# Kernel optimization log

Hardware: AMD Instinct MI355X
Metric: run time of the kernel (lower is better)

## Reference

```python
import jax, jax.numpy as jnp
from jax import lax
import numpy as np

C, CK, CV, K = 256, 32, 32, 3  # channels, key_channels, value_channels, kernel_size
B, H, W = 8, 128, 128


def setup_inputs() -> dict:
    key = jax.random.key(0)
    ks = jax.random.split(key, 12)
    s = 0.05
    return {
        "x": jax.random.normal(ks[0], (B, C, H, W), jnp.float32),
        # key branch: 1x1 conv C->CK (+ReLU), depthwise 3x3 CK->CK, 1x1 conv CK->K*K
        "k1_w": jax.random.normal(ks[1], (CK, C), jnp.float32) * s,
        "k1_b": jax.random.normal(ks[2], (CK,), jnp.float32) * s,
        "dw_w": jax.random.normal(ks[3], (CK, 1, K, K), jnp.float32) * s,
        "dw_b": jax.random.normal(ks[4], (CK,), jnp.float32) * s,
        "k3_w": jax.random.normal(ks[5], (K * K, CK), jnp.float32) * s,
        "k3_b": jax.random.normal(ks[6], (K * K,), jnp.float32) * s,
        # value branch: 1x1 conv C->CV (no act)
        "v_w": jax.random.normal(ks[7], (CV, C), jnp.float32) * s,
        "v_b": jax.random.normal(ks[8], (CV,), jnp.float32) * s,
        # out conv: 1x1 CV->C (no act)
        "o_w": jax.random.normal(ks[9], (C, CV), jnp.float32) * s,
        "o_b": jax.random.normal(ks[10], (C,), jnp.float32) * s,
    }


def _conv1x1(t, w, b):
    # t: [B,Cin,H,W], w: [Cout,Cin] -> [B,Cout,H,W]
    return jnp.einsum("bchw,oc->bohw", t, w) + b[None, :, None, None]


def reference(x, k1_w, k1_b, dw_w, dw_b, k3_w, k3_b, v_w, v_b, o_w, o_b):
    b, _, h, w = x.shape
    pad = (K - 1) // 2
    # ---- key branch ----
    k = jax.nn.relu(_conv1x1(x, k1_w, k1_b))
    k = lax.conv_general_dilated(
        k, dw_w, window_strides=(1, 1), padding=[(pad, pad), (pad, pad)],
        dimension_numbers=("NCHW", "OIHW", "NCHW"), feature_group_count=CK,
    ) + dw_b[None, :, None, None]
    k = _conv1x1(k, k3_w, k3_b)                      # [B, K*K, H, W]
    weights = jax.nn.softmax(k, axis=1)[:, None]     # [B, 1, K*K, H, W]
    # ---- value branch: 1x1 conv then unfold (3x3 neighborhoods, pad 1) ----
    v = _conv1x1(x, v_w, v_b)                        # [B, CV, H, W]
    vp = jnp.pad(v, ((0, 0), (0, 0), (pad, pad), (pad, pad)))
    # torch Unfold ordering: per-channel, kernel offsets row-major
    patches = jnp.stack(
        [vp[:, :, i : i + h, j : j + w] for i in range(K) for j in range(K)],
        axis=2,
    )                                                # [B, CV, K*K, H, W]
    y = jnp.sum(weights * patches, axis=2)           # [B, CV, H, W]
    y = _conv1x1(y, o_w, o_b)                        # [B, C, H, W]
    return x + y
```

## Files before the change

kernel.cpp:

```cpp
#include <hip/hip_runtime.h>
#include <cmath>

namespace {
constexpr int Cc = 256, CKc = 32, CVc = 32, KKc = 9;
constexpr int Bc = 8, Hc = 128, Wc = 128, HWc = Hc * Wc;

typedef __attribute__((ext_vector_type(8))) short   s16x8;
typedef __attribute__((ext_vector_type(8))) __bf16  bf16x8;
typedef __attribute__((ext_vector_type(4))) float   f32x4;

__device__ inline unsigned short f2bf(float f) {
    union { float f; unsigned u; } v; v.f = f;
    unsigned u = v.u + 0x7fffu + ((v.u >> 16) & 1u);
    return (unsigned short)(u >> 16);
}
}

__global__ __launch_bounds__(256) void ns_k1v(
    const float* __restrict__ x,
    const float* __restrict__ k1_w, const float* __restrict__ k1_b,
    const float* __restrict__ v_w,  const float* __restrict__ v_b,
    const float* __restrict__ o_w,
    unsigned short* __restrict__ k1pm, unsigned short* __restrict__ vpm,
    unsigned short* __restrict__ owbf)
{
    constexpr int LP = 72;
    __shared__ short w_bf[64][LP];
    __shared__ short x_bf[128][LP];

    const int tid = threadIdx.x;
    const int l   = tid & 63;
    const int li  = l & 15;
    const int lk  = l >> 4;
    const int wv  = __builtin_amdgcn_readfirstlane(tid >> 6);

    if (blockIdx.x == 0) {
        for (int i = tid * 4; i < Cc * CVc; i += 256 * 4) {
            const float4 f = *(const float4*)(o_w + i);
            const unsigned a = (unsigned)f2bf(f.x) | ((unsigned)f2bf(f.y) << 16);
            const unsigned c = (unsigned)f2bf(f.z) | ((unsigned)f2bf(f.w) << 16);
            *(uint2*)(owbf + i) = make_uint2(a, c);
        }
    }

    const int flat0 = blockIdx.x * 128;
    const int b  = flat0 / HWc;
    const int pp = flat0 - b * HWc;
    const float* xb = x + (size_t)b * Cc * HWc + pp;

    const int sp2 = (tid & 63) * 2;
    const int scg = tid >> 6;
    const int so   = tid & 63;
    const int swc0 = (tid >> 6) * 16;
    const float* wsrc = (so < 32) ? (k1_w + (size_t)so * Cc)
                                  : (v_w + (size_t)(so - 32) * Cc);

    f32x4 acc[8];
    const f32x4 zero = {0.f, 0.f, 0.f, 0.f};
#pragma unroll
    for (int i = 0; i < 8; ++i) acc[i] = zero;

    for (int c0 = 0; c0 < Cc; c0 += 64) {
        __syncthreads();
        {
            alignas(16) short tmp[16];
#pragma unroll
            for (int f = 0; f < 4; ++f) {
                const float4 fv = *(const float4*)(wsrc + c0 + swc0 + f * 4);
                tmp[f*4+0] = f2bf(fv.x); tmp[f*4+1] = f2bf(fv.y);
                tmp[f*4+2] = f2bf(fv.z); tmp[f*4+3] = f2bf(fv.w);
            }
            *(s16x8*)&w_bf[so][swc0]     = *(const s16x8*)&tmp[0];
            *(s16x8*)&w_bf[so][swc0 + 8] = *(const s16x8*)&tmp[8];
        }
        {
            float2 xv2[16];
#pragma unroll
            for (int cq = 0; cq < 16; ++cq)
                xv2[cq] = *(const float2*)(xb + (size_t)(c0 + scg * 16 + cq) * HWc + sp2);
            alignas(16) short ta[16], tb[16];
#pragma unroll
            for (int cq = 0; cq < 16; ++cq) {
                ta[cq] = f2bf(xv2[cq].x);
                tb[cq] = f2bf(xv2[cq].y);
            }
            *(s16x8*)&x_bf[sp2    ][scg * 16]     = *(const s16x8*)&ta[0];
            *(s16x8*)&x_bf[sp2    ][scg * 16 + 8] = *(const s16x8*)&ta[8];
            *(s16x8*)&x_bf[sp2 + 1][scg * 16]     = *(const s16x8*)&tb[0];
            *(s16x8*)&x_bf[sp2 + 1][scg * 16 + 8] = *(const s16x8*)&tb[8];
        }
        __syncthreads();

#pragma unroll
        for (int ks = 0; ks < 2; ++ks) {
            const s16x8 ar = *(const s16x8*)&w_bf[wv * 16 + li][ks * 32 + lk * 8];
            const bf16x8 af = __builtin_bit_cast(bf16x8, ar);
#pragma unroll
            for (int pt = 0; pt < 8; ++pt) {
                const s16x8 br = *(const s16x8*)&x_bf[pt * 16 + li][ks * 32 + lk * 8];
                acc[pt] = __builtin_amdgcn_mfma_f32_16x16x32_bf16(
                    af, __builtin_bit_cast(bf16x8, br), acc[pt], 0, 0, 0);
            }
        }
    }

    const bool is_k = wv < 2;
    const int obase = wv * 16 + lk * 4;
    const int chq = is_k ? obase : obase - 32;
    float bias[4];
#pragma unroll
    for (int r = 0; r < 4; ++r)
        bias[r] = is_k ? k1_b[obase + r] : v_b[obase + r - 32];
    unsigned short* dstb = is_k ? k1pm : vpm;

#pragma unroll
    for (int pt = 0; pt < 8; ++pt) {
        const size_t row = (size_t)b * HWc + pp + pt * 16 + li;
        float v0 = acc[pt][0] + bias[0], v1 = acc[pt][1] + bias[1];
        float v2 = acc[pt][2] + bias[2], v3 = acc[pt][3] + bias[3];
        if (is_k) {
            v0 = fmaxf(v0, 0.f); v1 = fmaxf(v1, 0.f);
            v2 = fmaxf(v2, 0.f); v3 = fmaxf(v3, 0.f);
        }
        const unsigned p01 = (unsigned)f2bf(v0) | ((unsigned)f2bf(v1) << 16);
        const unsigned p23 = (unsigned)f2bf(v2) | ((unsigned)f2bf(v3) << 16);
        *(uint2*)(dstb + row * 32 + chq) = make_uint2(p01, p23);
    }
}

__global__ __launch_bounds__(256) void ns_y(
    const unsigned short* __restrict__ k1pm,
    const unsigned short* __restrict__ vpm,
    const float* __restrict__ dw_w, const float* __restrict__ dw_b,
    const float* __restrict__ k3_w, const float* __restrict__ k3_b,
    unsigned short* __restrict__ ypm)
{
    __shared__ float plds[2][KKc][128];
    __shared__ float dwt[KKc][CKc];
    __shared__ float k3s[KKc][CKc];
    __shared__ float dwbs[CKc];
    __shared__ float k3bs[KKc];

    const int tid = threadIdx.x;
    if (tid < CKc * KKc) {
        const int ck = tid / KKc, kk = tid - ck * KKc;
        dwt[kk][ck] = dw_w[tid];
        ((float*)k3s)[tid] = k3_w[tid];
    }
    for (int idx = 256 + tid; idx < CKc * KKc; idx += 256) {
        const int ck = idx / KKc, kk = idx - ck * KKc;
        dwt[kk][ck] = dw_w[idx];
        ((float*)k3s)[idx] = k3_w[idx];
    }
    if (tid < CKc) dwbs[tid] = dw_b[tid];
    if (tid < KKc) k3bs[tid] = k3_b[tid];
    __syncthreads();

    const int bid = blockIdx.x;
    const int swz = (bid & 7) * 128 + (bid >> 3);

    const int pxi  = tid & 127;
    const int half = tid >> 7;
    const int cb   = half * 16;

    const int flat0 = swz * 128;
    const int b   = flat0 / HWc;
    const int row = flat0 - b * HWc;
    const int h   = row >> 7;
    const int w   = pxi;
    const int p   = row + pxi;

    const unsigned short* k1b = k1pm + (size_t)b * HWc * 32;
    const unsigned short* vb  = vpm  + (size_t)b * HWc * 32;

    float t[16];
#pragma unroll
    for (int e = 0; e < 16; ++e) t[e] = dwbs[cb + e];
#pragma unroll
    for (int i = 0; i < 3; ++i) {
        const int hh = h + i - 1;
#pragma unroll
        for (int j = 0; j < 3; ++j) {
            const int ww = w + j - 1;
            if (hh < 0 || hh >= Hc || ww < 0 || ww >= Wc) continue;
            const unsigned short* kr = k1b + (size_t)(hh * Wc + ww) * 32 + cb;
            const int ij = i * 3 + j;
#pragma unroll
            for (int qv = 0; qv < 2; ++qv) {
                const bf16x8 kv = __builtin_bit_cast(bf16x8, *(const s16x8*)(kr + qv * 8));
#pragma unroll
                for (int e = 0; e < 8; ++e)
                    t[qv * 8 + e] = fmaf((float)kv[e], dwt[ij][cb + qv * 8 + e],
                                         t[qv * 8 + e]);
            }
        }
    }

#pragma unroll
    for (int kk = 0; kk < KKc; ++kk) {
        float a = (half == 0) ? k3bs[kk] : 0.f;
#pragma unroll
        for (int e = 0; e < 16; ++e)
            a = fmaf(k3s[kk][cb + e], t[e], a);
        plds[half][kk][pxi] = a;
    }
    __syncthreads();

    float logit[KKc];
#pragma unroll
    for (int kk = 0; kk < KKc; ++kk)
        logit[kk] = plds[0][kk][pxi] + plds[1][kk][pxi];

    float m = logit[0];
#pragma unroll
    for (int kk = 1; kk < KKc; ++kk) m = fmaxf(m, logit[kk]);
    float s = 0.f;
#pragma unroll
    for (int kk = 0; kk < KKc; ++kk) { logit[kk] = expf(logit[kk] - m); s += logit[kk]; }
    const float inv = 1.f / s;
#pragma unroll
    for (int kk = 0; kk < KKc; ++kk) logit[kk] *= inv;

    float yv[16];
#pragma unroll
    for (int e = 0; e < 16; ++e) yv[e] = 0.f;
#pragma unroll
    for (int i = 0; i < 3; ++i) {
        const int hh = h + i - 1;
#pragma unroll
        for (int j = 0; j < 3; ++j) {
            const int ww = w + j - 1;
            if (hh < 0 || hh >= Hc || ww < 0 || ww >= Wc) continue;
            const unsigned short* vr = vb + (size_t)(hh * Wc + ww) * 32 + cb;
            const float wv = logit[i * 3 + j];
#pragma unroll
            for (int qv = 0; qv < 2; ++qv) {
                const bf16x8 vv = __builtin_bit_cast(bf16x8, *(const s16x8*)(vr + qv * 8));
#pragma unroll
                for (int e = 0; e < 8; ++e)
                    yv[qv * 8 + e] = fmaf(wv, (float)vv[e], yv[qv * 8 + e]);
            }
        }
    }

    alignas(16) short ybf[16];
#pragma unroll
    for (int e = 0; e < 16; ++e) ybf[e] = (short)f2bf(yv[e]);
    unsigned short* yo = ypm + ((size_t)b * HWc + p) * 32 + cb;
    *(float4*)(yo)     = *(const float4*)&ybf[0];
    *(float4*)(yo + 8) = *(const float4*)&ybf[8];
}

__global__ __launch_bounds__(256, 4) void ns_oconv(
    const float* __restrict__ x,
    const unsigned short* __restrict__ ypm,
    const unsigned short* __restrict__ owbf, const float* __restrict__ o_b,
    float* __restrict__ out)
{
    __shared__ float dlds[64 * 128];

    const int tid = threadIdx.x;
    const int w   = tid >> 6;
    const int l   = tid & 63;
    const int li  = l & 15;
    const int lk  = l >> 4;

    const int flat0 = blockIdx.x * 128;
    const int b  = flat0 / HWc;
    const int p0 = flat0 - b * HWc;

    const unsigned short* yb = ypm + ((size_t)b * HWc + p0) * 32;
    bf16x8 yfrag[8];
#pragma unroll
    for (int pt = 0; pt < 8; ++pt)
        yfrag[pt] = __builtin_bit_cast(bf16x8,
            *(const s16x8*)(yb + (size_t)(pt * 16 + li) * 32 + lk * 8));

    const float* xb0 = x + (size_t)b * Cc * HWc + p0;
    float* ob0 = out + (size_t)b * Cc * HWc + p0;

    for (int pass = 0; pass < 4; ++pass) {
        const int och0 = pass * 64;

        const int rowA = w * 16 + li;
        const bf16x8 wfrag = __builtin_bit_cast(bf16x8,
            *(const s16x8*)(owbf + (size_t)(och0 + rowA) * 32 + lk * 8));
        float* dro = dlds + rowA * 128;
        const int sw = (li & 7) << 2;
#pragma unroll
        for (int pt = 0; pt < 8; ++pt) {
            f32x4 acc = {0.f, 0.f, 0.f, 0.f};
            acc = __builtin_amdgcn_mfma_f32_16x16x32_bf16(yfrag[pt], wfrag, acc, 0, 0, 0);
            const int col = (pt * 16 + lk * 4) ^ sw;
            *(f32x4*)(dro + col) = acc;
        }

        float2 xvv[16];
#pragma unroll
        for (int r = 0; r < 16; ++r) {
            const int och = och0 + w * 16 + r;
            xvv[r] = *(const float2*)(xb0 + (size_t)och * HWc + l * 2);
        }
#pragma unroll
        for (int r = 0; r < 16; ++r) {
            const int row = w * 16 + r;
            const int och = och0 + row;
            const float bi = o_b[och];
            const int col = (l * 2) ^ ((row & 7) << 2);
            const float2 dv = *(const float2*)(dlds + row * 128 + col);
            float2 ov = { xvv[r].x + dv.x + bi, xvv[r].y + dv.y + bi };
            *(float2*)(ob0 + (size_t)och * HWc + l * 2) = ov;
        }
    }
}

extern "C" void kernel_launch(void* const* d_in, const int* in_sizes, int n_in,
                              void* d_out, int out_size, void* d_ws, size_t ws_size,
                              hipStream_t stream)
{
    const float* x    = (const float*)d_in[0];
    const float* k1_w = (const float*)d_in[1];
    const float* k1_b = (const float*)d_in[2];
    const float* dw_w = (const float*)d_in[3];
    const float* dw_b = (const float*)d_in[4];
    const float* k3_w = (const float*)d_in[5];
    const float* k3_b = (const float*)d_in[6];
    const float* v_w  = (const float*)d_in[7];
    const float* v_b  = (const float*)d_in[8];
    const float* o_w  = (const float*)d_in[9];
    const float* o_b  = (const float*)d_in[10];
    float* out = (float*)d_out;

    unsigned short* k1pm = (unsigned short*)d_ws;
    unsigned short* vpm  = k1pm + (size_t)Bc * HWc * 32;
    unsigned short* ypm  = vpm  + (size_t)Bc * HWc * 32;
    unsigned short* owbf = ypm  + (size_t)Bc * HWc * 32;

    const int npx = Bc * HWc;

    ns_k1v  <<<dim3(npx / 128), dim3(256), 0, stream>>>(x, k1_w, k1_b, v_w, v_b, o_w,
                                                        k1pm, vpm, owbf);
    ns_y    <<<dim3(npx / 128), dim3(256), 0, stream>>>(k1pm, vpm, dw_w, dw_b,
                                                        k3_w, k3_b, ypm);
    ns_oconv<<<dim3(npx / 128), dim3(256), 0, stream>>>(x, ypm, owbf, o_b, out);
}
```

Baseline: 90.61 us.

## Fuse attention-weighted aggregation with output 1x1 conv via shared memory

Merges the kernel computing the softmax-weighted 3x3 value aggregation with the output 1x1 conv kernel. The bf16 y tile now goes through LDS (padded stride 40) instead of a global round trip, which removes one launch and the write and re-read of an 8x16384x32 bf16 buffer. The fused kernel also uses the swizzled block order from ns_y for the oconv stage and reuses one LDS buffer for logits, y and the conv output. In exchange it adds barriers and raises register and LDS pressure under launch bounds of 4 blocks.

```diff
diff --git a/kernel.cpp b/kernel.cpp
--- a/kernel.cpp
+++ b/kernel.cpp
@@ -128,26 +128,25 @@
     }
 }
 
-__global__ __launch_bounds__(256) void ns_y(
+__global__ __launch_bounds__(256, 4) void ns_yoc(
+    const float* __restrict__ x,
     const unsigned short* __restrict__ k1pm,
     const unsigned short* __restrict__ vpm,
     const float* __restrict__ dw_w, const float* __restrict__ dw_b,
     const float* __restrict__ k3_w, const float* __restrict__ k3_b,
-    unsigned short* __restrict__ ypm)
+    const unsigned short* __restrict__ owbf, const float* __restrict__ o_b,
+    float* __restrict__ out)
 {
-    __shared__ float plds[2][KKc][128];
+    __shared__ alignas(16) float dlds[64 * 128];
+    float* plds = dlds;
+    short* ylds = (short*)(dlds + 2 * KKc * 128);
     __shared__ float dwt[KKc][CKc];
     __shared__ float k3s[KKc][CKc];
     __shared__ float dwbs[CKc];
     __shared__ float k3bs[KKc];
 
     const int tid = threadIdx.x;
-    if (tid < CKc * KKc) {
-        const int ck = tid / KKc, kk = tid - ck * KKc;
-        dwt[kk][ck] = dw_w[tid];
-        ((float*)k3s)[tid] = k3_w[tid];
-    }
-    for (int idx = 256 + tid; idx < CKc * KKc; idx += 256) {
+    for (int idx = tid; idx < CKc * KKc; idx += 256) {
         const int ck = idx / KKc, kk = idx - ck * KKc;
         dwt[kk][ck] = dw_w[idx];
         ((float*)k3s)[idx] = k3_w[idx];
@@ -168,7 +167,6 @@
     const int row = flat0 - b * HWc;
     const int h   = row >> 7;
     const int w   = pxi;
-    const int p   = row + pxi;
 
     const unsigned short* k1b = k1pm + (size_t)b * HWc * 32;
     const unsigned short* vb  = vpm  + (size_t)b * HWc * 32;
@@ -202,14 +200,14 @@
 #pragma unroll
         for (int e = 0; e < 16; ++e)
             a = fmaf(k3s[kk][cb + e], t[e], a);
-        plds[half][kk][pxi] = a;
+        plds[(half * KKc + kk) * 128 + pxi] = a;
     }
     __syncthreads();
 
     float logit[KKc];
 #pragma unroll
     for (int kk = 0; kk < KKc; ++kk)
-        logit[kk] = plds[0][kk][pxi] + plds[1][kk][pxi];
+        logit[kk] = plds[kk * 128 + pxi] + plds[(KKc + kk) * 128 + pxi];
 
     float m = logit[0];
 #pragma unroll
@@ -243,46 +241,35 @@
         }
     }
 
-    alignas(16) short ybf[16];
-#pragma unroll
-    for (int e = 0; e < 16; ++e) ybf[e] = (short)f2bf(yv[e]);
-    unsigned short* yo = ypm + ((size_t)b * HWc + p) * 32 + cb;
-    *(float4*)(yo)     = *(const float4*)&ybf[0];
-    *(float4*)(yo + 8) = *(const float4*)&ybf[8];
-}
-
-__global__ __launch_bounds__(256, 4) void ns_oconv(
-    const float* __restrict__ x,
-    const unsigned short* __restrict__ ypm,
-    const unsigned short* __restrict__ owbf, const float* __restrict__ o_b,
-    float* __restrict__ out)
-{
-    __shared__ float dlds[64 * 128];
-
-    const int tid = threadIdx.x;
-    const int w   = tid >> 6;
+    {
+        alignas(16) short ybf[16];
+#pragma unroll
+        for (int e = 0; e < 16; ++e) ybf[e] = (short)f2bf(yv[e]);
+        short* yo = ylds + pxi * 40 + cb;
+        *(float4*)(yo)     = *(const float4*)&ybf[0];
+        *(float4*)(yo + 8) = *(const float4*)&ybf[8];
+    }
+    __syncthreads();
+
+    const int wv2 = tid >> 6;
     const int l   = tid & 63;
     const int li  = l & 15;
     const int lk  = l >> 4;
 
-    const int flat0 = blockIdx.x * 128;
-    const int b  = flat0 / HWc;
-    const int p0 = flat0 - b * HWc;
-
-    const unsigned short* yb = ypm + ((size_t)b * HWc + p0) * 32;
     bf16x8 yfrag[8];
 #pragma unroll
     for (int pt = 0; pt < 8; ++pt)
         yfrag[pt] = __builtin_bit_cast(bf16x8,
-            *(const s16x8*)(yb + (size_t)(pt * 16 + li) * 32 + lk * 8));
-
-    const float* xb0 = x + (size_t)b * Cc * HWc + p0;
-    float* ob0 = out + (size_t)b * Cc * HWc + p0;
+            *(const s16x8*)(ylds + (pt * 16 + li) * 40 + lk * 8));
+    __syncthreads();
+
+    const float* xb0 = x + (size_t)b * Cc * HWc + row;
+    float* ob0 = out + (size_t)b * Cc * HWc + row;
 
     for (int pass = 0; pass < 4; ++pass) {
         const int och0 = pass * 64;
 
-        const int rowA = w * 16 + li;
+        const int rowA = wv2 * 16 + li;
         const bf16x8 wfrag = __builtin_bit_cast(bf16x8,
             *(const s16x8*)(owbf + (size_t)(och0 + rowA) * 32 + lk * 8));
         float* dro = dlds + rowA * 128;
@@ -298,16 +285,16 @@
         float2 xvv[16];
 #pragma unroll
         for (int r = 0; r < 16; ++r) {
-            const int och = och0 + w * 16 + r;
+            const int och = och0 + wv2 * 16 + r;
             xvv[r] = *(const float2*)(xb0 + (size_t)och * HWc + l * 2);
         }
 #pragma unroll
         for (int r = 0; r < 16; ++r) {
-            const int row = w * 16 + r;
-            const int och = och0 + row;
+            const int rw = wv2 * 16 + r;
+            const int och = och0 + rw;
             const float bi = o_b[och];
-            const int col = (l * 2) ^ ((row & 7) << 2);
-            const float2 dv = *(const float2*)(dlds + row * 128 + col);
+            const int col = (l * 2) ^ ((rw & 7) << 2);
+            const float2 dv = *(const float2*)(dlds + rw * 128 + col);
             float2 ov = { xvv[r].x + dv.x + bi, xvv[r].y + dv.y + bi };
             *(float2*)(ob0 + (size_t)och * HWc + l * 2) = ov;
         }
@@ -333,14 +320,12 @@
 
     unsigned short* k1pm = (unsigned short*)d_ws;
     unsigned short* vpm  = k1pm + (size_t)Bc * HWc * 32;
-    unsigned short* ypm  = vpm  + (size_t)Bc * HWc * 32;
-    unsigned short* owbf = ypm  + (size_t)Bc * HWc * 32;
+    unsigned short* owbf = vpm  + (size_t)Bc * HWc * 32;
 
     const int npx = Bc * HWc;
 
-    ns_k1v  <<<dim3(npx / 128), dim3(256), 0, stream>>>(x, k1_w, k1_b, v_w, v_b, o_w,
-                                                        k1pm, vpm, owbf);
-    ns_y    <<<dim3(npx / 128), dim3(256), 0, stream>>>(k1pm, vpm, dw_w, dw_b,
-                                                        k3_w, k3_b, ypm);
-    ns_oconv<<<dim3(npx / 128), dim3(256), 0, stream>>>(x, ypm, owbf, o_b, out);
-}
+    ns_k1v<<<dim3(npx / 128), dim3(256), 0, stream>>>(x, k1_w, k1_b, v_w, v_b, o_w,
+                                                      k1pm, vpm, owbf);
+    ns_yoc<<<dim3(npx / 128), dim3(256), 0, stream>>>(x, k1pm, vpm, dw_w, dw_b,
+                                                      k3_w, k3_b, owbf, o_b, out);
+}
```

Result: faster. 82.63 us (-8.8%).
